# Kernel tuning notes

Hardware: AMD Instinct MI355X
Metric: run time of the kernel (lower is better)

Reference implementation:

```python
import jax, jax.numpy as jnp
import numpy as np


def _mha(q, k, v, num_heads):
    # q,k,v: [B, L, C] -> multi-head attention, scale = 1/sqrt(head_dim)
    B, Lq, C = q.shape
    Lk = k.shape[1]
    d = C // num_heads
    qh = q.reshape(B, Lq, num_heads, d)
    kh = k.reshape(B, Lk, num_heads, d)
    vh = v.reshape(B, Lk, num_heads, d)
    scale = 1.0 / jnp.sqrt(jnp.asarray(d, q.dtype))
    scores = jnp.einsum('blhd,bmhd->bhlm', qh, kh) * scale
    probs = jax.nn.softmax(scores, axis=-1)
    out = jnp.einsum('bhlm,bmhd->blhd', probs, vh)
    return out.reshape(B, Lq, C)


def setup_inputs() -> dict:
    key = jax.random.key(0)
    ks = jax.random.split(key, 9)
    b, n, f, l, C = 1, 4, 8, 256, 320
    s = 0.02
    return {
        'hidden_states': jax.random.normal(ks[0], (b * n * f, l, C), jnp.float32),
        'Wq': jax.random.normal(ks[1], (C, C), jnp.float32) * s,
        'Wk': jax.random.normal(ks[2], (C, C), jnp.float32) * s,
        'Wv': jax.random.normal(ks[3], (C, C), jnp.float32) * s,
        'Wo': jax.random.normal(ks[4], (C, C), jnp.float32) * s,
        'bo': jnp.zeros((C,), jnp.float32),
        'Wq_i2v': jax.random.normal(ks[5], (C, C), jnp.float32) * s,
        'Wo_i2v': jax.random.normal(ks[6], (C, C), jnp.float32) * s,
        'bo_i2v': jnp.zeros((C,), jnp.float32),
        'num_heads': 8,
        'num_views': 4,
        'num_frames': 8,
    }


def reference(hidden_states, Wq, Wk, Wv, Wo, bo, Wq_i2v, Wo_i2v, bo_i2v,
              num_heads, num_views, num_frames):
    BNF, l, C = hidden_states.shape
    n, f = num_views, num_frames
    b = BNF // (n * f)
    # '(b n f) l c -> (b f) (n l) c'
    h = hidden_states.reshape(b, n, f, l, C).transpose(0, 2, 1, 3, 4).reshape(b * f, n * l, C)
    L = n * l

    q = h @ Wq
    k = h @ Wk
    v = h @ Wv

    # first-frame KV broadcast across all frames within the same b
    k_first = jnp.broadcast_to(k.reshape(b, f, L, C)[:, 0:1], (b, f, L, C)).reshape(b * f, L, C)
    v_first = jnp.broadcast_to(v.reshape(b, f, L, C)[:, 0:1], (b, f, L, C)).reshape(b * f, L, C)

    base = _mha(q, k, v, num_heads)

    q_i2v = h @ Wq_i2v
    i2v = _mha(q_i2v, k_first, v_first, num_heads)
    i2v = i2v @ Wo_i2v + bo_i2v

    out = (base + i2v) @ Wo + bo

    # '(b f) (n l) c -> (b n f) l c'
    out = out.reshape(b, f, n, l, C).transpose(0, 2, 1, 3, 4).reshape(b * n * f, l, C)
    return out
```

## Files before the change

kernel.cpp:

```cpp
#include <hip/hip_runtime.h>
#include <hip/hip_bf16.h>

#define MROWS 8192
#define CDIM  320
#define QPAD  512

typedef __attribute__((ext_vector_type(8))) short bf16x8;
typedef __attribute__((ext_vector_type(4))) float f32x4;

__device__ __forceinline__ unsigned bfbits(float x) {
  union { float f; unsigned u; } a; a.f = x;
  return a.u + 0x8000u;
}
__device__ __forceinline__ void splitbf(float x, short& hi, short& lo) {
  unsigned hu = bfbits(x) & 0xffff0000u;
  union { unsigned u; float f; } h; h.u = hu;
  hi = (short)(hu >> 16);
  lo = (short)(bfbits(x - h.f) >> 16);
}
__device__ __forceinline__ unsigned pk_bf16(float a, float b) {
  union { __hip_bfloat162 h2; unsigned u; } cv;
  cv.h2 = __float22bfloat162_rn(float2{a, b});
  return cv.u;
}

__device__ __forceinline__ void cp16_g2l(const void* g, void* l) {
  __builtin_amdgcn_global_load_lds(
      (const __attribute__((address_space(1))) void*)g,
      (__attribute__((address_space(3))) void*)l, 16, 0, 0);
}

__device__ __forceinline__ int swizzle_row(int r) {
  int ff = r >> 10;
  int t  = r & 1023;
  int nn = t >> 8;
  int ll = t & 255;
  return nn * 2048 + ff * 256 + ll;
}

__global__ __launch_bounds__(256) void wc_kernel(
    const float* __restrict__ Woi, const float* __restrict__ Wo,
    float* __restrict__ Wc)
{
  const int r0 = blockIdx.x * 64, c0 = blockIdx.y * 64;
  __shared__ float As[64][36];
  __shared__ float Bs[32][68];
  const int tid = threadIdx.x, tx = tid & 15, ty = tid >> 4;
  float acc[4][4] = {};

  const int ra = tid >> 3, kq = (tid & 7) * 4;
  const int kb = tid >> 4, cq = (tid & 15) * 4;

  for (int k0 = 0; k0 < 320; k0 += 32) {
    float4 a1 = *(const float4*)(Woi + (size_t)(r0 + ra) * 320 + k0 + kq);
    float4 a2 = *(const float4*)(Woi + (size_t)(r0 + ra + 32) * 320 + k0 + kq);
    float4 b1 = *(const float4*)(Wo + (size_t)(k0 + kb) * 320 + c0 + cq);
    float4 b2 = *(const float4*)(Wo + (size_t)(k0 + kb + 16) * 320 + c0 + cq);
    __syncthreads();
    *(float4*)&As[ra][kq] = a1;
    *(float4*)&As[ra + 32][kq] = a2;
    *(float4*)&Bs[kb][cq] = b1;
    *(float4*)&Bs[kb + 16][cq] = b2;
    __syncthreads();
    #pragma unroll
    for (int kk = 0; kk < 32; ++kk) {
      float4 bv = *(const float4*)&Bs[kk][tx * 4];
      #pragma unroll
      for (int i = 0; i < 4; ++i) {
        float a = As[ty * 4 + i][kk];
        acc[i][0] = fmaf(a, bv.x, acc[i][0]);
        acc[i][1] = fmaf(a, bv.y, acc[i][1]);
        acc[i][2] = fmaf(a, bv.z, acc[i][2]);
        acc[i][3] = fmaf(a, bv.w, acc[i][3]);
      }
    }
  }
  #pragma unroll
  for (int i = 0; i < 4; ++i) {
    float4 v = make_float4(acc[i][0], acc[i][1], acc[i][2], acc[i][3]);
    *(float4*)(Wc + (size_t)(r0 + ty * 4 + i) * 320 + c0 + tx * 4) = v;
  }
}

__global__ __launch_bounds__(256) void pack_kernel(
    const float* __restrict__ hidden,
    const float* __restrict__ Wq, const float* __restrict__ Wk,
    const float* __restrict__ Wv, const float* __restrict__ Wqi,
    const float* __restrict__ Wo, const float* __restrict__ Wc,
    const float* __restrict__ bo, const float* __restrict__ boi,
    short* __restrict__ Ah, short* __restrict__ Al,
    short* __restrict__ WTh, short* __restrict__ WTl,
    short* __restrict__ WFh, short* __restrict__ WFl,
    float* __restrict__ bc,
    short* __restrict__ Qp, short* __restrict__ Kp, short* __restrict__ Qip,
    float qscale)
{
  const int b = blockIdx.x, tid = threadIdx.x;
  if (b < 64) {
    const int r0 = b * 128;
    for (int e = tid; e < 128 * 80; e += 256) {
      int r = e / 80, cq = (e % 80) * 4;
      float4 x = *(const float4*)(hidden + (size_t)swizzle_row(r0 + r) * 320 + cq);
      union { ushort4 v; short s[4]; } h, l;
      splitbf(x.x, h.s[0], l.s[0]); splitbf(x.y, h.s[1], l.s[1]);
      splitbf(x.z, h.s[2], l.s[2]); splitbf(x.w, h.s[3], l.s[3]);
      *(ushort4*)&Ah[(size_t)(r0 + r) * 320 + cq] = h.v;
      *(ushort4*)&Al[(size_t)(r0 + r) * 320 + cq] = l.v;
    }
  } else if (b < 128) {
    const int t2 = b - 64, wi = t2 >> 4, seg = t2 & 15;
    const float* W = wi == 0 ? Wq : wi == 1 ? Wk : wi == 2 ? Wv : Wqi;
    const float s = (wi == 0 || wi == 3) ? qscale : 1.0f;
    short* th = WTh + (size_t)wi * 320 * 320;
    short* tl = WTl + (size_t)wi * 320 * 320;
    for (int e = tid; e < 20 * 320; e += 256) {
      int n = seg * 20 + e / 320, k = e % 320;
      short hi, lo;
      splitbf(W[(size_t)k * 320 + n] * s, hi, lo);
      th[(size_t)n * 320 + k] = hi;
      tl[(size_t)n * 320 + k] = lo;
    }
  } else if (b < 160) {
    const int t2 = b - 128;
    for (int e = tid; e < 10 * 640; e += 256) {
      int n = t2 * 10 + e / 640, k = e % 640;
      float x = (k < 320) ? Wo[(size_t)k * 320 + n] : Wc[(size_t)(k - 320) * 320 + n];
      short hi, lo;
      splitbf(x, hi, lo);
      WFh[(size_t)n * 640 + k] = hi;
      WFl[(size_t)n * 640 + k] = lo;
    }
  } else if (b < 168) {
    const int n = (b - 160) * 40 + tid;
    if (tid < 40) {
      float s = bo[n];
      for (int j = 0; j < 320; ++j) s = fmaf(boi[j], Wo[(size_t)j * 320 + n], s);
      bc[n] = s;
    }
  } else {
    const int bz = b - 168, buf = bz >> 5, seg = bz & 31;
    short* P = buf == 0 ? Qp : buf == 1 ? Kp : Qip;
    const uint4 z = make_uint4(0, 0, 0, 0);
    for (int e = tid; e < 256 * 24; e += 256) {
      int row = (seg << 8) + (e / 24);
      int cc = e % 24, h = cc / 3, c3 = cc % 3;
      *(uint4*)&P[(size_t)row * QPAD + h * 64 + 40 + c3 * 8] = z;
    }
  }
}

__global__ __launch_bounds__(256, 3) void mfma_gemm(
    const short* __restrict__ Ah, const short* __restrict__ Al,
    const short* __restrict__ BTh, const short* __restrict__ BTl,
    int K, int mode,
    short* __restrict__ Qp, short* __restrict__ Kp,
    short* __restrict__ Vt, short* __restrict__ Qip,
    float* __restrict__ Of, const float* __restrict__ bias)
{
  const int tid  = threadIdx.x;
  const int wave = tid >> 6;
  const int lane = tid & 63;
  const int quad = lane >> 4;
  const int l16  = lane & 15;
  const int row0 = blockIdx.x * 128;

  const short *bth, *btl;
  int nbase, wi = 0;
  if (mode == 0) {
    const int ct = blockIdx.y;
    wi = ct / 5;
    bth = BTh + (size_t)wi * 320 * 320;
    btl = BTl + (size_t)wi * 320 * 320;
    nbase = (ct % 5) * 64;
  } else {
    bth = BTh; btl = BTl;
    nbase = blockIdx.y * 64;
  }

  __shared__ short Ash[128][32], Asl[128][32];
  __shared__ short Bsh[64][32],  Bsl[64][32];

  f32x4 acc[2][4];
  #pragma unroll
  for (int mt = 0; mt < 2; ++mt)
    #pragma unroll
    for (int nt = 0; nt < 4; ++nt) acc[mt][nt] = (f32x4){0.f, 0.f, 0.f, 0.f};

  const int lr = lane >> 2, lc = (lane & 3) * 8;
  const short* gah = Ah + (size_t)(row0 + wave * 16 + lr) * K + lc;
  const short* gal = Al ? Al + (size_t)(row0 + wave * 16 + lr) * K + lc : nullptr;
  const short* gbh = bth + (size_t)(nbase + wave * 16 + lr) * K + lc;
  const short* gbl = btl + (size_t)(nbase + wave * 16 + lr) * K + lc;
  short* lah1 = &Ash[wave * 16][0];
  short* lah2 = &Ash[64 + wave * 16][0];
  short* lal1 = &Asl[wave * 16][0];
  short* lal2 = &Asl[64 + wave * 16][0];
  short* lbh  = &Bsh[wave * 16][0];
  short* lbl  = &Bsl[wave * 16][0];

  for (int k0 = 0; k0 < K; k0 += 32) {
    __syncthreads();
    cp16_g2l(gah + k0, lah1);
    cp16_g2l(gah + (size_t)64 * K + k0, lah2);
    if (Al) {
      cp16_g2l(gal + k0, lal1);
      cp16_g2l(gal + (size_t)64 * K + k0, lal2);
    }
    cp16_g2l(gbh + k0, lbh);
    cp16_g2l(gbl + k0, lbl);
    __syncthreads();

    bf16x8 afh[2], afl[2], bfh[4], bfl[4];
    #pragma unroll
    for (int mt = 0; mt < 2; ++mt) {
      afh[mt] = *(const bf16x8*)&Ash[wave * 32 + mt * 16 + l16][quad * 8];
      if (Al) afl[mt] = *(const bf16x8*)&Asl[wave * 32 + mt * 16 + l16][quad * 8];
    }
    #pragma unroll
    for (int nt = 0; nt < 4; ++nt) {
      bfh[nt] = *(const bf16x8*)&Bsh[nt * 16 + l16][quad * 8];
      bfl[nt] = *(const bf16x8*)&Bsl[nt * 16 + l16][quad * 8];
    }
    #pragma unroll
    for (int mt = 0; mt < 2; ++mt)
      #pragma unroll
      for (int nt = 0; nt < 4; ++nt) {
        acc[mt][nt] = __builtin_amdgcn_mfma_f32_16x16x32_bf16(afh[mt], bfh[nt], acc[mt][nt], 0, 0, 0);
        acc[mt][nt] = __builtin_amdgcn_mfma_f32_16x16x32_bf16(afh[mt], bfl[nt], acc[mt][nt], 0, 0, 0);
        if (Al)
          acc[mt][nt] = __builtin_amdgcn_mfma_f32_16x16x32_bf16(afl[mt], bfh[nt], acc[mt][nt], 0, 0, 0);
      }
  }

  if (mode == 0) {
    if (wi == 2) {
      #pragma unroll
      for (int mt = 0; mt < 2; ++mt)
        #pragma unroll
        for (int nt = 0; nt < 4; ++nt) {
          const int col  = nbase + nt * 16 + l16;
          const int rowb = row0 + wave * 32 + mt * 16 + quad * 4;
          union { ushort4 v; short s[4]; } pk;
          #pragma unroll
          for (int r = 0; r < 4; ++r) pk.s[r] = (short)(bfbits(acc[mt][nt][r]) >> 16);
          *(ushort4*)&Vt[(size_t)col * MROWS + rowb] = pk.v;
        }
    } else {
      short* Op = wi == 0 ? Qp : wi == 1 ? Kp : Qip;
      #pragma unroll
      for (int mt = 0; mt < 2; ++mt)
        #pragma unroll
        for (int nt = 0; nt < 4; ++nt) {
          const int col  = nbase + nt * 16 + l16;
          const int h    = col / 40;
          const int pcol = h * 64 + (col - h * 40);
          const int rowb = row0 + wave * 32 + mt * 16 + quad * 4;
          #pragma unroll
          for (int r = 0; r < 4; ++r)
            Op[(size_t)(rowb + r) * QPAD + pcol] = (short)(bfbits(acc[mt][nt][r]) >> 16);
        }
    }
  } else {
    #pragma unroll
    for (int mt = 0; mt < 2; ++mt)
      #pragma unroll
      for (int nt = 0; nt < 4; ++nt) {
        const int col  = nbase + nt * 16 + l16;
        const int rowb = row0 + wave * 32 + mt * 16 + quad * 4;
        const float bb = bias[col];
        #pragma unroll
        for (int r = 0; r < 4; ++r)
          Of[(size_t)swizzle_row(rowb + r) * CDIM + col] = acc[mt][nt][r] + bb;
      }
  }
}

__global__ __launch_bounds__(256, 4) void attn_kernel(
    const short* __restrict__ Qp, const short* __restrict__ Qip,
    const short* __restrict__ Kp, const short* __restrict__ Vtg,
    short* __restrict__ AOh)
{
  const int qblk = blockIdx.x;
  const int hh   = blockIdx.y;
  const int zz   = blockIdx.z;
  const int var  = zz >> 3;
  const int bf   = zz & 7;
  const int tid  = threadIdx.x;
  const int wave = tid >> 6;
  const int lane = tid & 63;
  const int quad = lane >> 4;
  const int l16  = lane & 15;

  const short* Q = var ? Qip : Qp;
  const int kvbase = var ? 0 : (bf << 10);
  const int coff = var * 320 + hh * 40;

  __shared__ short Ks[64][64];
  __shared__ short Vt[48][64];
  __shared__ short Ps[4][16][68];

  if (tid < 64) {
    const int pr = tid >> 3;
    uint4 fill = (pr == 0) ? make_uint4(0x3F803F80u, 0x3F803F80u, 0x3F803F80u, 0x3F803F80u)
                           : make_uint4(0, 0, 0, 0);
    *(uint4*)&Vt[40 + pr][(tid & 7) * 8] = fill;
  }

  bf16x8 qf0[2], qf1[2];
  #pragma unroll
  for (int qt = 0; qt < 2; ++qt) {
    const short* qp = Q + (size_t)((bf << 10) + (qblk << 7) + (wave << 5) + (qt << 4) + l16) * QPAD + hh * 64;
    qf0[qt] = *(const bf16x8*)(qp + quad * 8);
    qf1[qt] = *(const bf16x8*)(qp + 32 + quad * 8);
  }

  f32x4 acc[2][3];
  #pragma unroll
  for (int qt = 0; qt < 2; ++qt)
    #pragma unroll
    for (int t = 0; t < 3; ++t) acc[qt][t] = (f32x4){0.f, 0.f, 0.f, 0.f};

  const short* Kb = Kp + (size_t)kvbase * QPAD + hh * 64;
  const short* Vb = Vtg + (size_t)(hh * 40) * MROWS + kvbase;

  const int lrow = lane >> 3;
  const int gch  = ((lane & 7) ^ (lrow & 7)) * 8;
  const int sw   = l16 & 7;

  for (int s0 = 0; s0 < 1024; s0 += 64) {
    __syncthreads();
    #pragma unroll
    for (int j = 0; j < 4; ++j) {
      const int u = j * 4 + wave;
      if (u < 8) {
        cp16_g2l(Kb + (size_t)(s0 + u * 8 + lrow) * QPAD + gch, &Ks[u * 8][0]);
      } else if (u < 13) {
        cp16_g2l(Vb + (size_t)((u - 8) * 8 + lrow) * MROWS + s0 + gch, &Vt[(u - 8) * 8][0]);
      }
    }
    __syncthreads();

    bf16x8 vf[2][3];
    #pragma unroll
    for (int kh = 0; kh < 2; ++kh)
      #pragma unroll
      for (int t = 0; t < 3; ++t)
        vf[kh][t] = *(const bf16x8*)&Vt[t * 16 + l16][((kh * 4 + quad) ^ sw) * 8];

    #pragma unroll
    for (int qt = 0; qt < 2; ++qt) {
      #pragma unroll
      for (int kt = 0; kt < 4; ++kt) {
        const short* kr = &Ks[kt * 16 + l16][0];
        bf16x8 kb0 = *(const bf16x8*)(kr + (quad ^ sw) * 8);
        bf16x8 kb1 = *(const bf16x8*)(kr + ((quad + 4) ^ sw) * 8);
        f32x4 st = (f32x4){0.f, 0.f, 0.f, 0.f};
        st = __builtin_amdgcn_mfma_f32_16x16x32_bf16(kb0, qf0[qt], st, 0, 0, 0);
        st = __builtin_amdgcn_mfma_f32_16x16x32_bf16(kb1, qf1[qt], st, 0, 0, 0);
        float p0 = __builtin_amdgcn_exp2f(st[0]);
        float p1 = __builtin_amdgcn_exp2f(st[1]);
        float p2 = __builtin_amdgcn_exp2f(st[2]);
        float p3 = __builtin_amdgcn_exp2f(st[3]);
        uint2 pk;
        pk.x = pk_bf16(p0, p1);
        pk.y = pk_bf16(p2, p3);
        *(uint2*)&Ps[wave][l16][kt * 16 + quad * 4] = pk;
      }

      asm volatile("s_waitcnt lgkmcnt(0)" ::: "memory");

      bf16x8 pa0 = *(const bf16x8*)&Ps[wave][l16][quad * 8];
      bf16x8 pa1 = *(const bf16x8*)&Ps[wave][l16][32 + quad * 8];
      #pragma unroll
      for (int t = 0; t < 3; ++t) {
        acc[qt][t] = __builtin_amdgcn_mfma_f32_16x16x32_bf16(pa0, vf[0][t], acc[qt][t], 0, 0, 0);
        acc[qt][t] = __builtin_amdgcn_mfma_f32_16x16x32_bf16(pa1, vf[1][t], acc[qt][t], 0, 0, 0);
      }
    }
  }

  #pragma unroll
  for (int qt = 0; qt < 2; ++qt) {
    float invr[4];
    #pragma unroll
    for (int r = 0; r < 4; ++r) {
      float d = __shfl(acc[qt][2][r], quad * 16 + 8, 64);
      invr[r] = 1.f / d;
    }

    const int baserow = (bf << 10) + (qblk << 7) + (wave << 5) + (qt << 4) + quad * 4;
    #pragma unroll
    for (int t = 0; t < 3; ++t) {
      int dcol = t * 16 + l16;
      if (dcol < 40) {
        short* op = AOh + (size_t)baserow * 640 + coff + dcol;
        #pragma unroll
        for (int r = 0; r < 4; ++r)
          op[(size_t)r * 640] = (short)(bfbits(acc[qt][t][r] * invr[r]) >> 16);
      }
    }
  }
}

extern "C" void kernel_launch(void* const* d_in, const int* in_sizes, int n_in,
                              void* d_out, int out_size, void* d_ws, size_t ws_size,
                              hipStream_t stream) {
  const float* hidden  = (const float*)d_in[0];
  const float* Wq      = (const float*)d_in[1];
  const float* Wk      = (const float*)d_in[2];
  const float* Wv      = (const float*)d_in[3];
  const float* Wo      = (const float*)d_in[4];
  const float* bo      = (const float*)d_in[5];
  const float* Wq_i2v  = (const float*)d_in[6];
  const float* Wo_i2v  = (const float*)d_in[7];
  const float* bo_i2v  = (const float*)d_in[8];
  float* out = (float*)d_out;

  const size_t SZ  = (size_t)MROWS * CDIM;
  const size_t SZP = (size_t)MROWS * QPAD;
  short* Ah  = (short*)d_ws;
  short* Al  = Ah + SZ;
  short* AOh = Ah;
  short* Qp  = Al + SZ;
  short* Kp  = Qp + SZP;
  short* Qip = Kp + SZP;
  short* Vt  = Qip + SZP;
  short* WTh = Vt + (size_t)328 * MROWS;
  short* WTl = WTh + 409600;
  short* WFh = WTl + 409600;
  short* WFl = WFh + 204800;
  float* Wc  = (float*)(WFl + 204800);
  float* bc  = Wc + 102400;

  const float qscale = 0.22811011717177393f;

  wc_kernel<<<dim3(5, 5), 256, 0, stream>>>(Wo_i2v, Wo, Wc);

  pack_kernel<<<dim3(264), 256, 0, stream>>>(
      hidden, Wq, Wk, Wv, Wq_i2v, Wo, Wc, bo, bo_i2v,
      Ah, Al, WTh, WTl, WFh, WFl, bc, Qp, Kp, Qip, qscale);

  mfma_gemm<<<dim3(64, 20), 256, 0, stream>>>(
      Ah, Al, WTh, WTl, 320, 0, Qp, Kp, Vt, Qip, nullptr, nullptr);

  attn_kernel<<<dim3(8, 8, 16), 256, 0, stream>>>(Qp, Qip, Kp, Vt, AOh);

  mfma_gemm<<<dim3(64, 5), 256, 0, stream>>>(
      AOh, nullptr, WFh, WFl, 640, 1, nullptr, nullptr, nullptr, nullptr, out, bc);
}
```

Before: 201.5 us.

## Double-buffer K/V tiles in attention, flatten grid, add MFMA priority hints

Adds two LDS buffers for the K and V tiles in the attention kernel so the async global-to-LDS copy of the next 64-key tile is issued before computing the current one, and drops one barrier per tile. The grid becomes 1D, with query-block index as the slowest dimension, which changes block dispatch order and may improve K/V cache locality. s_setprio is raised around the MFMA sequences. LDS use grows by about 14 KB per block, which may reduce occupancy at the declared launch bounds.

```diff
diff --git a/kernel.cpp b/kernel.cpp
--- a/kernel.cpp
+++ b/kernel.cpp
@@ -280,9 +280,11 @@
     const short* __restrict__ Kp, const short* __restrict__ Vtg,
     short* __restrict__ AOh)
 {
-  const int qblk = blockIdx.x;
-  const int hh   = blockIdx.y;
-  const int zz   = blockIdx.z;
+  const int lid  = blockIdx.x;
+  const int qblk = lid >> 7;
+  const int t7   = lid & 127;
+  const int hh   = t7 & 7;
+  const int zz   = t7 >> 3;
   const int var  = zz >> 3;
   const int bf   = zz & 7;
   const int tid  = threadIdx.x;
@@ -295,15 +297,16 @@
   const int kvbase = var ? 0 : (bf << 10);
   const int coff = var * 320 + hh * 40;
 
-  __shared__ short Ks[64][64];
-  __shared__ short Vt[48][64];
+  __shared__ short Ks[2][64][64];
+  __shared__ short Vt[2][48][64];
   __shared__ short Ps[4][16][68];
 
-  if (tid < 64) {
-    const int pr = tid >> 3;
+  if (tid < 128) {
+    const int bsel = tid >> 6, t6 = tid & 63;
+    const int pr = t6 >> 3;
     uint4 fill = (pr == 0) ? make_uint4(0x3F803F80u, 0x3F803F80u, 0x3F803F80u, 0x3F803F80u)
                            : make_uint4(0, 0, 0, 0);
-    *(uint4*)&Vt[40 + pr][(tid & 7) * 8] = fill;
+    *(uint4*)&Vt[bsel][40 + pr][(t6 & 7) * 8] = fill;
   }
 
   bf16x8 qf0[2], qf1[2];
@@ -327,36 +330,38 @@
   const int gch  = ((lane & 7) ^ (lrow & 7)) * 8;
   const int sw   = l16 & 7;
 
-  for (int s0 = 0; s0 < 1024; s0 += 64) {
-    __syncthreads();
+  auto stage = [&](int s0, int bsel) {
     #pragma unroll
     for (int j = 0; j < 4; ++j) {
       const int u = j * 4 + wave;
       if (u < 8) {
-        cp16_g2l(Kb + (size_t)(s0 + u * 8 + lrow) * QPAD + gch, &Ks[u * 8][0]);
+        cp16_g2l(Kb + (size_t)(s0 + u * 8 + lrow) * QPAD + gch, &Ks[bsel][u * 8][0]);
       } else if (u < 13) {
-        cp16_g2l(Vb + (size_t)((u - 8) * 8 + lrow) * MROWS + s0 + gch, &Vt[(u - 8) * 8][0]);
-      }
-    }
-    __syncthreads();
-
+        cp16_g2l(Vb + (size_t)((u - 8) * 8 + lrow) * MROWS + s0 + gch, &Vt[bsel][(u - 8) * 8][0]);
+      }
+    }
+  };
+
+  auto compute = [&](int bsel) {
     bf16x8 vf[2][3];
     #pragma unroll
     for (int kh = 0; kh < 2; ++kh)
       #pragma unroll
       for (int t = 0; t < 3; ++t)
-        vf[kh][t] = *(const bf16x8*)&Vt[t * 16 + l16][((kh * 4 + quad) ^ sw) * 8];
+        vf[kh][t] = *(const bf16x8*)&Vt[bsel][t * 16 + l16][((kh * 4 + quad) ^ sw) * 8];
 
     #pragma unroll
     for (int qt = 0; qt < 2; ++qt) {
       #pragma unroll
       for (int kt = 0; kt < 4; ++kt) {
-        const short* kr = &Ks[kt * 16 + l16][0];
+        const short* kr = &Ks[bsel][kt * 16 + l16][0];
         bf16x8 kb0 = *(const bf16x8*)(kr + (quad ^ sw) * 8);
         bf16x8 kb1 = *(const bf16x8*)(kr + ((quad + 4) ^ sw) * 8);
         f32x4 st = (f32x4){0.f, 0.f, 0.f, 0.f};
+        __builtin_amdgcn_s_setprio(1);
         st = __builtin_amdgcn_mfma_f32_16x16x32_bf16(kb0, qf0[qt], st, 0, 0, 0);
         st = __builtin_amdgcn_mfma_f32_16x16x32_bf16(kb1, qf1[qt], st, 0, 0, 0);
+        __builtin_amdgcn_s_setprio(0);
         float p0 = __builtin_amdgcn_exp2f(st[0]);
         float p1 = __builtin_amdgcn_exp2f(st[1]);
         float p2 = __builtin_amdgcn_exp2f(st[2]);
@@ -371,12 +376,27 @@
 
       bf16x8 pa0 = *(const bf16x8*)&Ps[wave][l16][quad * 8];
       bf16x8 pa1 = *(const bf16x8*)&Ps[wave][l16][32 + quad * 8];
+      __builtin_amdgcn_s_setprio(1);
       #pragma unroll
       for (int t = 0; t < 3; ++t) {
         acc[qt][t] = __builtin_amdgcn_mfma_f32_16x16x32_bf16(pa0, vf[0][t], acc[qt][t], 0, 0, 0);
         acc[qt][t] = __builtin_amdgcn_mfma_f32_16x16x32_bf16(pa1, vf[1][t], acc[qt][t], 0, 0, 0);
       }
-    }
+      __builtin_amdgcn_s_setprio(0);
+    }
+  };
+
+  stage(0, 0);
+  __syncthreads();
+
+  #pragma unroll 1
+  for (int s0 = 0; s0 < 1024; s0 += 128) {
+    stage(s0 + 64, 1);
+    compute(0);
+    __syncthreads();
+    if (s0 + 128 < 1024) stage(s0 + 128, 0);
+    compute(1);
+    __syncthreads();
   }
 
   #pragma unroll
@@ -443,7 +463,7 @@
   mfma_gemm<<<dim3(64, 20), 256, 0, stream>>>(
       Ah, Al, WTh, WTl, 320, 0, Qp, Kp, Vt, Qip, nullptr, nullptr);
 
-  attn_kernel<<<dim3(8, 8, 16), 256, 0, stream>>>(Qp, Qip, Kp, Vt, AOh);
+  attn_kernel<<<dim3(1024), 256, 0, stream>>>(Qp, Qip, Kp, Vt, AOh);
 
   mfma_gemm<<<dim3(64, 5), 256, 0, stream>>>(
       AOh, nullptr, WFh, WFl, 640, 1, nullptr, nullptr, nullptr, nullptr, out, bc);
```

New measurement: 202.0 us. About the same (+0.3%).
